# Performance work log

Hardware: AMD Instinct MI355X
Metric: run time of the kernel (lower is better)

The kernel has to match this reference:

```python
import jax, jax.numpy as jnp
import numpy as np
from jax import lax

V, E, H, MEL = 256, 512, 1024, 128
B, T_TXT, T_MEL = 128, 256, 800
BN_EPS = 1e-5


def setup_inputs() -> dict:
    key = jax.random.key(0)
    ks = jax.random.split(key, 32)
    s = 0.05
    n = jax.random.normal
    inp = {
        "x": jax.random.randint(ks[0], (B, T_TXT), 0, V),
        "text_seq_lens": jax.random.randint(ks[1], (B,), 1, T_TXT + 1),
        "y": n(ks[2], (B, T_MEL, MEL), jnp.float32),
        "mel_spec_lens": jax.random.randint(ks[3], (B,), 1, T_MEL + 1),
        # encoder params
        "emb": n(ks[4], (V, E)) * s,
        "enc_lin_W": n(ks[5], (E, E)) * s,
        "enc_lin_b": jnp.zeros((E,)),
        "conv1_W": n(ks[6], (E, E, 3)) * s,
        "conv1_b": jnp.zeros((E,)),
        "bn1_g": 1.0 + n(ks[7], (E,)) * s,
        "bn1_b": n(ks[8], (E,)) * s,
        "conv2_W": n(ks[9], (E, E, 3)) * s,
        "conv2_b": jnp.zeros((E,)),
        "bn2_g": 1.0 + n(ks[10], (E,)) * s,
        "bn2_b": n(ks[11], (E,)) * s,
        # encoder LSTM (torch gate order i,f,g,o); b = b_ih + b_hh fused
        "Wih_e": n(ks[12], (4 * H, E)) * s,
        "Whh_e": n(ks[13], (4 * H, H)) * s,
        "b_e": n(ks[14], (4 * H,)) * 0.01,
        # decoder LSTM
        "Wih_d": n(ks[15], (4 * H, MEL)) * s,
        "Whh_d": n(ks[16], (4 * H, H)) * s,
        "b_d": n(ks[17], (4 * H,)) * 0.01,
        # output projections
        "Wp": n(ks[18], (MEL, H)) * s,
        "bp": jnp.zeros((MEL,)),
        "Wg": n(ks[19], (1, H)) * s,
        "bg": jnp.zeros((1,)),
    }
    return inp


def lstm_step(xt, h, c, Wih, Whh, b):
    g = xt @ Wih.T + h @ Whh.T + b  # [B, 4H]
    i, f, gg, o = jnp.split(g, 4, axis=-1)
    c2 = jax.nn.sigmoid(f) * c + jax.nn.sigmoid(i) * jnp.tanh(gg)
    h2 = jax.nn.sigmoid(o) * jnp.tanh(c2)
    return h2, c2


def reference(x, text_seq_lens, y, mel_spec_lens, emb, enc_lin_W, enc_lin_b,
              conv1_W, conv1_b, bn1_g, bn1_b, conv2_W, conv2_b, bn2_g, bn2_b,
              Wih_e, Whh_e, b_e, Wih_d, Whh_d, b_d, Wp, bp, Wg, bg):
    Bq, Ttxt = x.shape
    Tmel = y.shape[1]
    dt = y.dtype

    def conv_bn_relu(h, W, b, g, beta):
        h = lax.conv_general_dilated(h, W, (1,), ((1, 1),),
                                     dimension_numbers=("NCH", "OIH", "NCH"))
        h = h + b[None, :, None]
        # BN in eval mode: running_mean=0, running_var=1
        h = g[None, :, None] * (h / jnp.sqrt(1.0 + BN_EPS)) + beta[None, :, None]
        return jax.nn.relu(h)  # dropout is identity in eval

    e = emb[x]                                  # [B,T,E]
    e = e @ enc_lin_W.T + enc_lin_b
    h = e.transpose(0, 2, 1)                    # [B,E,T]
    h = conv_bn_relu(h, conv1_W, conv1_b, bn1_g, bn1_b)
    h = conv_bn_relu(h, conv2_W, conv2_b, bn2_g, bn2_b)
    h = h.transpose(0, 2, 1)                    # [B,T,E]

    # encoder LSTM with pack_padded semantics: state frozen past seq len,
    # so final (h,c) is the state at each sequence's true last step.
    valid = jnp.arange(Ttxt)[:, None] < text_seq_lens[None, :]  # [T,B]

    def enc_step(carry, inp):
        hh, cc = carry
        xt, v = inp
        h2, c2 = lstm_step(xt, hh, cc, Wih_e, Whh_e, b_e)
        v = v[:, None]
        return (jnp.where(v, h2, hh), jnp.where(v, c2, cc)), None

    z = jnp.zeros((Bq, H), dt)
    (hS, cS), _ = lax.scan(enc_step, (z, z), (h.transpose(1, 0, 2), valid))

    def dec_step(carry, _):
        hh, cc, inp = carry
        h2, c2 = lstm_step(inp, hh, cc, Wih_d, Whh_d, b_d)
        mel = h2 @ Wp.T + bp           # [B,MEL]
        gate = (h2 @ Wg.T + bg)[:, 0]  # [B]
        return (h2, c2, mel), (mel, gate)

    sos = jnp.zeros((Bq, MEL), dt)
    _, (mels, gates) = lax.scan(dec_step, (hS, cS, sos), None, length=Tmel)
    mels = mels.transpose(1, 0, 2)   # [B,Tmel,MEL]
    gates = gates.T                  # [B,Tmel]

    mask = jnp.arange(Tmel)[None, :] > mel_spec_lens[:, None]  # strict > as in source
    masked_mel = jnp.where(mask[:, :, None], jnp.zeros((), dt), mels)
    masked_gate = jnp.where(mask, jnp.asarray(1000.0, dt), gates)
    return masked_mel, masked_gate, mask
```

## Files before the change

### kernel.cpp

```cpp
#include <hip/hip_runtime.h>
#include <math.h>

#define BB 128
#define TT 256
#define TMEL 800
#define EE 512
#define HH 1024
#define MELD 128
#define VV 256

#define OFF_PROJ  0u
#define OFF_T1    131072u
#define OFF_WR2   524288u
#define OFF_BB1   1310720u
#define OFF_BB2   1311232u
#define OFF_B2    1311744u
#define OFF_W2C   1315840u
#define OFF_BAR   5510144u
#define OFF_WENCR 5522688u
#define OFF_WIHS  7619840u
#define OFF_W2CR  8668416u
#define OFF_WHHDS 10765568u
#define OFF_WPGS  12862720u
#define OFF_H2B   12936448u
#define OFF_RING  21325056u

typedef __bf16 bfv8 __attribute__((ext_vector_type(8)));
typedef float f32x4 __attribute__((ext_vector_type(4)));
typedef unsigned u32x4 __attribute__((ext_vector_type(4)));

__device__ __forceinline__ unsigned short f2b(float f){
  union { float f; unsigned u; } v; v.f = f;
  unsigned u = v.u;
  return (unsigned short)((u + 0x7fffu + ((u>>16)&1u)) >> 16);
}
__device__ __forceinline__ float sigm(float x){ return 1.0f/(1.0f+expf(-x)); }

__device__ __forceinline__ f32x4 mfma16(bfv8 a, bfv8 b, f32x4 c){
  return __builtin_amdgcn_mfma_f32_16x16x32_bf16(a, b, c, 0, 0, 0);
}


__global__ void k_proj(const float* __restrict__ emb, const float* __restrict__ W,
                       const float* __restrict__ bias, float* __restrict__ proj){
  __shared__ float er[EE];
  int v = blockIdx.x;
  for(int i=threadIdx.x;i<EE;i+=256) er[i]=emb[v*EE+i];
  __syncthreads();
  for(int e=threadIdx.x;e<EE;e+=256){
    const float* wr = W + e*EE;
    float acc=0.f;
    for(int k=0;k<EE;k+=4){
      float4 w4 = *(const float4*)(wr+k);
      acc += er[k]*w4.x + er[k+1]*w4.y + er[k+2]*w4.z + er[k+3]*w4.w;
    }
    proj[v*EE+e] = acc + bias[e];
  }
}

__global__ void k_t1(const float* __restrict__ proj, const float* __restrict__ W1,
                     const float* __restrict__ g1, float* __restrict__ T1){
  __shared__ float pr[EE];
  int v = blockIdx.x; int k3 = blockIdx.y;
  for(int i=threadIdx.x;i<EE;i+=256) pr[i]=proj[v*EE+i];
  __syncthreads();
  const float s = rsqrtf(1.f+1e-5f);
  for(int c=threadIdx.x;c<EE;c+=256){
    float acc=0.f;
    const float* w = W1 + c*EE*3 + k3;
    for(int ci=0;ci<EE;ci++) acc += pr[ci]*w[ci*3];
    T1[(v*3+k3)*EE+c] = g1[c]*s*acc;
  }
}

__global__ void k_wr2(const float* __restrict__ W2, const float* __restrict__ g2,
                      unsigned short* __restrict__ Wr){
  int idx = blockIdx.x*256+threadIdx.x;
  if(idx >= EE*3*EE) return;
  int c = idx/1536; int r = idx%1536; int k3 = r/EE; int ci = r%EE;
  const float s = rsqrtf(1.f+1e-5f);
  Wr[idx] = f2b(g2[c]*s*W2[(c*EE+ci)*3+k3]);
}

__global__ void k_bb(const float* __restrict__ b1,const float* __restrict__ g1,const float* __restrict__ be1,
                     const float* __restrict__ b2,const float* __restrict__ g2,const float* __restrict__ be2,
                     float* __restrict__ bb1, float* __restrict__ bb2){
  int c = threadIdx.x + blockIdx.x*256; if(c>=EE) return;
  const float s = rsqrtf(1.f+1e-5f);
  bb1[c] = g1[c]*s*b1[c] + be1[c];
  bb2[c] = g2[c]*s*b2[c] + be2[c];
}

__global__ void k_b2(const float* __restrict__ bd, const float* __restrict__ Wih,
                     const float* __restrict__ bp, float* __restrict__ b2){
  int j = blockIdx.x*256+threadIdx.x; if(j>=4096) return;
  float acc = bd[j];
  const float* w = Wih + j*MELD;
  for(int m=0;m<MELD;m++) acc += w[m]*bp[m];
  b2[j] = acc;
}

__global__ void k_w2c(const float* __restrict__ Whh, const float* __restrict__ Wih,
                      const float* __restrict__ Wp, float* __restrict__ W2c){
  __shared__ float wl[8][MELD];
  int j0 = blockIdx.x*8; int k = blockIdx.y*256 + threadIdx.x;
  for(int i=threadIdx.x;i<8*MELD;i+=256) wl[i/MELD][i%MELD] = Wih[(j0+i/MELD)*MELD + (i%MELD)];
  __syncthreads();
  float acc[8];
  #pragma unroll
  for(int jj=0;jj<8;jj++) acc[jj]=Whh[(j0+jj)*HH+k];
  for(int m=0;m<MELD;m++){
    float wp = Wp[m*HH+k];
    #pragma unroll
    for(int jj=0;jj<8;jj++) acc[jj] += wl[jj][m]*wp;
  }
  #pragma unroll
  for(int jj=0;jj<8;jj++) W2c[(j0+jj)*HH+k] = acc[jj];
}

__global__ void k_pack(const float* __restrict__ src, unsigned short* __restrict__ dst,
                       int NKT, int K){
  int tile = blockIdx.x;
  int cg = tile>>3, wv = tile&7;
  int tot = NKT*64*8;
  for(int i=threadIdx.x; i<tot; i+=256){
    int kt = i>>9; int l = (i>>3)&63; int e = i&7;
    int j = (wv>>1)*1024 + cg*32 + (wv&1)*16 + (l&15);
    int k = ((l>>4)<<3) + kt*32 + e;
    dst[((size_t)(tile*NKT + kt)*64 + l)*8 + e] = f2b(src[(size_t)j*K + k]);
  }
}

__global__ void k_pack_pg(const float* __restrict__ Wp, const float* __restrict__ Wg,
                          unsigned short* __restrict__ dst){
  int nt = blockIdx.x;
  for(int i=threadIdx.x; i<32*64*8; i+=256){
    int kt = i>>9; int l = (i>>3)&63; int e = i&7;
    int n = nt*16 + (l&15);
    int k = ((l>>4)<<3) + kt*32 + e;
    float v = (n<MELD)? Wp[(size_t)n*HH+k] : (n==MELD? Wg[k] : 0.f);
    dst[((size_t)(nt*32 + kt)*64 + l)*8 + e] = f2b(v);
  }
}


__global__ void k_pad(unsigned short* __restrict__ h1pb){
  int idx = blockIdx.x*256+threadIdx.x;
  int c = idx & 511; int b = idx >> 9;
  h1pb[((size_t)b*258)*EE + c] = 0;
  h1pb[((size_t)b*258 + 257)*EE + c] = 0;
}

__global__ void k_conv1(const int* __restrict__ x, const float* __restrict__ T1,
                        const float* __restrict__ bb1, unsigned short* __restrict__ h1pb){
  int idx = blockIdx.x*256+threadIdx.x;
  int c = idx & 511; int bt = idx >> 9; int t = bt & 255; int b = bt >> 8;
  float acc = bb1[c];
  if(t > 0)    acc += T1[(size_t)(x[b*TT+t-1]*3+0)*EE+c];
               acc += T1[(size_t)(x[b*TT+t  ]*3+1)*EE+c];
  if(t < TT-1) acc += T1[(size_t)(x[b*TT+t+1]*3+2)*EE+c];
  h1pb[((size_t)b*258 + t + 1)*EE + c] = f2b(fmaxf(acc, 0.f));
}

template<int NKT>
__device__ __forceinline__ void mm_seg_stream(const unsigned short* A, int lda,
    const unsigned short* Wrow, f32x4& acc0, f32x4& acc1, int l, int wv){
  int r0 = wv*32 + (l&15);
  int k8 = (l>>4)*8;
  const unsigned short* a0 = A + (size_t)r0*lda + k8;
  const unsigned short* a1 = a0 + 16*lda;
  const unsigned short* wp = Wrow + k8;
  #pragma unroll
  for(int kt=0;kt<NKT;kt++){
    bfv8 bv = *(const bfv8*)(const void*)(wp + kt*32);
    acc0 = mfma16(*(const bfv8*)(const void*)(a0 + kt*32), bv, acc0);
    acc1 = mfma16(*(const bfv8*)(const void*)(a1 + kt*32), bv, acc1);
  }
}

__global__ __launch_bounds__(256,2) void k_conv2mm(const unsigned short* __restrict__ h1pb,
    const unsigned short* __restrict__ Wr2b, const float* __restrict__ bb2,
    unsigned short* __restrict__ h2b){
  int b = blockIdx.x;
  int th = blockIdx.y;
  int nt = blockIdx.z;
  int tid=threadIdx.x; int wv=tid>>6, l=tid&63;
  const unsigned short* A = h1pb + ((size_t)b*258 + th*128)*EE;
  const unsigned short* Wrow = Wr2b + (size_t)(nt*16+(l&15))*1536;
  f32x4 acc0={0,0,0,0}, acc1={0,0,0,0};
  mm_seg_stream<48>(A, EE, Wrow, acc0, acc1, l, wv);
  int rr=(l>>4)*4, cc=l&15;
  int n = nt*16+cc;
  float bias = bb2[n];
  #pragma unroll
  for(int mi=0;mi<2;mi++){
    f32x4 acc = mi?acc1:acc0;
    int tb = th*128 + wv*32 + mi*16 + rr;
    #pragma unroll
    for(int q=0;q<4;q++){
      float v = fmaxf(acc[q]+bias, 0.f);
      h2b[((size_t)(tb+q)*BB + b)*EE + n] = f2b(v);
    }
  }
}

__device__ __forceinline__ unsigned l2_poll(unsigned* p){
  unsigned v;
  asm volatile("global_atomic_add %0, %1, %2, off sc0\n\ts_waitcnt vmcnt(0)"
               : "=v"(v) : "v"(p), "v"(0u) : "memory");
  return v;
}

__device__ __forceinline__ void g_arrive(unsigned* cnt_slow, unsigned* gen_slow,
                                         unsigned* cnt_fast, unsigned* bcast_base,
                                         bool fastp){
  __syncthreads();
  if(threadIdx.x == 0){
    if(fastp){
      unsigned old = __hip_atomic_fetch_add(cnt_fast, 1u, __ATOMIC_RELAXED, __HIP_MEMORY_SCOPE_WORKGROUP);
      if((old & 31u) == 31u){
        unsigned g = (old + 1u) >> 5;
        #pragma unroll
        for(int i=0;i<32;i++)
          __hip_atomic_store(bcast_base + i*32, g, __ATOMIC_RELAXED, __HIP_MEMORY_SCOPE_WORKGROUP);
      }
    } else {
      unsigned old = __hip_atomic_fetch_add(cnt_slow, 1u, __ATOMIC_RELAXED, __HIP_MEMORY_SCOPE_AGENT);
      if(old == 31u){
        __hip_atomic_store(cnt_slow, 0u, __ATOMIC_RELAXED, __HIP_MEMORY_SCOPE_AGENT);
        __hip_atomic_fetch_add(gen_slow, 1u, __ATOMIC_RELAXED, __HIP_MEMORY_SCOPE_AGENT);
      }
    }
  }
}
__device__ __forceinline__ void g_wait(unsigned* gen_slow, unsigned* mybcast,
                                       unsigned ge, bool fastp){
  if(threadIdx.x == 0){
    if(fastp){
      while(l2_poll(mybcast) < ge) __builtin_amdgcn_s_sleep(1);
    } else {
      while(__hip_atomic_load(gen_slow, __ATOMIC_RELAXED, __HIP_MEMORY_SCOPE_AGENT) < ge)
        __builtin_amdgcn_s_sleep(1);
    }
  }
  asm volatile("" ::: "memory");
  __syncthreads();
}

__device__ __forceinline__ void h_store(unsigned int* ptr, unsigned int val, bool fastp){
  if(fastp) __hip_atomic_store(ptr, val, __ATOMIC_RELAXED, __HIP_MEMORY_SCOPE_WORKGROUP);
  else      __hip_atomic_store(ptr, val, __ATOMIC_RELAXED, __HIP_MEMORY_SCOPE_AGENT);
}
__device__ __forceinline__ void h_store64(unsigned long long* ptr, unsigned long long val, bool fastp){
  if(fastp) __hip_atomic_store(ptr, val, __ATOMIC_RELAXED, __HIP_MEMORY_SCOPE_WORKGROUP);
  else      __hip_atomic_store(ptr, val, __ATOMIC_RELAXED, __HIP_MEMORY_SCOPE_AGENT);
}

__device__ __forceinline__ void stage_h(unsigned short* hs, const unsigned short* slotp,
                                        int bg, int tid, bool fastp){
  if(fastp){
    const char* base = (const char*)(slotp + (size_t)(bg*16)*HH);
    #pragma unroll
    for(int jj=0;jj<2;jj++){
      int i0 = tid + (jj*2+0)*512, i1 = tid + (jj*2+1)*512;
      int r0 = i0>>7, c0 = i0&127, r1 = i1>>7, c1 = i1&127;
      int o0 = r0*2048 + c0*16,     o1 = r1*2048 + c1*16;
      u32x4 v0, v1;
      asm volatile(
        "global_load_dwordx4 %0, %2, off sc0\n\t"
        "global_load_dwordx4 %1, %3, off sc0\n\t"
        "s_waitcnt vmcnt(0)"
        : "=&v"(v0), "=&v"(v1)
        : "v"(base + o0), "v"(base + o1)
        : "memory");
      *(u32x4*)((char*)hs + (o0 ^ ((r0&7)<<4))) = v0;
      *(u32x4*)((char*)hs + (o1 ^ ((r1&7)<<4))) = v1;
    }
  } else {
    for(int i = tid; i < 4096; i += 512){
      int r = i >> 8, c8 = i & 255;
      const unsigned long long* p =
        (const unsigned long long*)(slotp + (size_t)(bg*16+r)*HH + c8*4);
      unsigned long long v = __hip_atomic_load(p, __ATOMIC_RELAXED, __HIP_MEMORY_SCOPE_AGENT);
      *(unsigned long long*)((char*)hs + ((r*2048 + c8*8) ^ ((r&7)<<4))) = v;
    }
  }
}

__global__ __launch_bounds__(512,1) void k_recur(
  const unsigned short* __restrict__ h2b, unsigned short* __restrict__ ring,
  const unsigned short* __restrict__ WencR, const unsigned short* __restrict__ WihS,
  const unsigned short* __restrict__ W2cR, const unsigned short* __restrict__ WhhdS,
  const unsigned short* __restrict__ WpgS,
  const float* __restrict__ bhe, const float* __restrict__ bd, const float* __restrict__ b2,
  const float* __restrict__ bp, const float* __restrict__ bgp,
  unsigned int* __restrict__ bar,
  const int* __restrict__ tlen, const int* __restrict__ mlen,
  float* __restrict__ outmel, float* __restrict__ outgate)
{
  __shared__ __align__(16) unsigned short hs[16*1024];
  __shared__ __align__(16) unsigned short Xs[16*512];
  __shared__ float Gs[16][132];
  __shared__ unsigned s_ids[32];
  __shared__ int s_fast;

  const int bid = blockIdx.x;
  const int bg = bid & 7, cg = bid >> 3;
  const int tid = threadIdx.x;
  const int wvi = tid >> 6, l = tid & 63;
  const int tile = cg*8 + wvi;
  unsigned int* cnt_slow = bar + bg*32;
  unsigned int* gen_slow = bar + 256 + bg*32;
  unsigned int* xtab     = bar + 512;
  unsigned int* cnt_fast = bar + 1024 + bg*32;
  unsigned int* bcastb   = bar + 2048 + bg*1024;
  unsigned int* mybcast  = bcastb + cg*32;
  unsigned int ge = 0;

  if(tid == 0){
    unsigned id;
    asm volatile("s_getreg_b32 %0, hwreg(HW_REG_XCC_ID)" : "=s"(id));
    __hip_atomic_store(xtab + bid, id + 1u, __ATOMIC_RELAXED, __HIP_MEMORY_SCOPE_AGENT);
  }
  if(tid < 32){
    unsigned v;
    do {
      v = __hip_atomic_load(xtab + (tid*8 + bg), __ATOMIC_RELAXED, __HIP_MEMORY_SCOPE_AGENT);
    } while(v == 0u);
    s_ids[tid] = v;
  }
  __syncthreads();
  if(tid == 0){
    int f = 1;
    for(int i=1;i<32;i++) if(s_ids[i] != s_ids[0]) f = 0;
    s_fast = f;
  }
  __syncthreads();
  const bool fastp = (s_fast != 0);

  const int fr = l & 15;
  const int hswz = (fr & 7) << 4;
  const int hbase = fr*2048 + ((l>>4)<<4);
  const int xbase = fr*1024 + ((l>>4)<<4);

  const int lr = tid >> 4;
  const int lc = (tid & 15) * 2;
  const int hcol = cg*32 + lc;
  float cs0 = 0.f, cs1 = 0.f;
  unsigned int hp = 0u;
  int mylen = 0;
  if(tid < 256) mylen = tlen[bg*16 + lr];

  if(tid < 128){
    int r = tid >> 3, c4 = (tid & 7) * 4;
    unsigned long long* p = (unsigned long long*)
      (ring + (size_t)100*BB*HH + (size_t)(bg*16+r)*HH + cg*32 + c4);
    h_store64(p, 0ull, fastp);
  }
  ge++; g_arrive(cnt_slow, gen_slow, cnt_fast, bcastb, fastp);

  f32x4 bw[32];

  {
    const f32x4* wsrc = (const f32x4*)(const void*)(WencR + ((size_t)(tile*32)*64 + l)*8);
    #pragma unroll
    for(int kt=0;kt<32;kt++) bw[kt] = wsrc[kt*64];
    #pragma unroll
    for(int kt=0;kt<32;kt++) asm volatile("" : "+v"(bw[kt]));
  }

  float ei0=0,ei1=0,ef0=0,ef1=0,eg0=0,eg1=0,eo0=0,eo1=0;
  if(tid < 256){
    ei0=bhe[hcol];      ei1=bhe[hcol+1];
    ef0=bhe[HH+hcol];   ef1=bhe[HH+hcol+1];
    eg0=bhe[2*HH+hcol]; eg1=bhe[2*HH+hcol+1];
    eo0=bhe[3*HH+hcol]; eo1=bhe[3*HH+hcol+1];
  }

  #pragma unroll 1
  for(int t=0;t<TT;t++){
    {
      const uint4* src = (const uint4*)(h2b + (size_t)(t*BB + bg*16)*EE);
      for(int i = tid; i < 1024; i += 512){
        int r = i >> 6, c16 = i & 63;
        uint4 v = src[r*64 + c16];
        *(uint4*)((char*)Xs + ((r*1024 + c16*16) ^ ((r&7)<<4))) = v;
      }
    }
    __syncthreads();
    f32x4 a0 = {0.f,0.f,0.f,0.f}, a1 = {0.f,0.f,0.f,0.f};
    {
      const unsigned short* wsrc = WihS + (size_t)tile*16*64*8;
      #pragma unroll
      for(int kt=0;kt<16;kt+=2){
        bfv8 wf0 = *(const bfv8*)(const void*)(wsrc + ((size_t)kt*64 + l)*8);
        bfv8 wf1 = *(const bfv8*)(const void*)(wsrc + ((size_t)(kt+1)*64 + l)*8);
        bfv8 xv0 = *(const bfv8*)(const void*)((const char*)Xs + ((xbase + kt*64) ^ hswz));
        bfv8 xv1 = *(const bfv8*)(const void*)((const char*)Xs + ((xbase + (kt+1)*64) ^ hswz));
        a0 = mfma16(xv0, wf0, a0);
        a1 = mfma16(xv1, wf1, a1);
      }
    }
    g_wait(gen_slow, mybcast, ge, fastp);
    stage_h(hs, ring + (size_t)(100 + (t&1))*BB*HH, bg, tid, fastp);
    __syncthreads();
    #pragma unroll
    for(int kt=0;kt<32;kt+=2){
      bfv8 hv0 = *(const bfv8*)(const void*)((const char*)hs + ((hbase + kt*64) ^ hswz));
      bfv8 hv1 = *(const bfv8*)(const void*)((const char*)hs + ((hbase + (kt+1)*64) ^ hswz));
      a0 = mfma16(hv0, __builtin_bit_cast(bfv8, bw[kt]), a0);
      a1 = mfma16(hv1, __builtin_bit_cast(bfv8, bw[kt+1]), a1);
    }
    {
      f32x4 acc = a0 + a1;
      int rr = (l>>4)*4;
      #pragma unroll
      for(int q=0;q<4;q++) Gs[rr+q][wvi*16 + fr] = acc[q];
    }
    __syncthreads();
    if(tid < 256){
      float gi0 = Gs[lr][lc]    + ei0, gi1 = Gs[lr][lc+1] + ei1;
      float gf0 = Gs[lr][32+lc] + ef0, gf1 = Gs[lr][33+lc] + ef1;
      float gg0 = Gs[lr][64+lc] + eg0, gg1 = Gs[lr][65+lc] + eg1;
      float go0 = Gs[lr][96+lc] + eo0, go1 = Gs[lr][97+lc] + eo1;
      float c20 = sigm(gf0)*cs0 + sigm(gi0)*tanhf(gg0);
      float c21 = sigm(gf1)*cs1 + sigm(gi1)*tanhf(gg1);
      float h20 = sigm(go0)*tanhf(c20);
      float h21 = sigm(go1)*tanhf(c21);
      if(t < mylen){
        cs0 = c20; cs1 = c21;
        hp = (unsigned)f2b(h20) | ((unsigned)f2b(h21)<<16);
      }
      unsigned short* outslot = (t==TT-1) ? (ring + (size_t)99*BB*HH)
                                          : (ring + (size_t)(100 + ((t+1)&1))*BB*HH);
      h_store((unsigned int*)(outslot + (size_t)(bg*16+lr)*HH + hcol), hp, fastp);
    }
    ge++; g_arrive(cnt_slow, gen_slow, cnt_fast, bcastb, fastp);
  }

  {
    const f32x4* wsrc = (const f32x4*)(const void*)(W2cR + ((size_t)(tile*32)*64 + l)*8);
    #pragma unroll
    for(int kt=0;kt<32;kt++) bw[kt] = wsrc[kt*64];
    #pragma unroll
    for(int kt=0;kt<32;kt++) asm volatile("" : "+v"(bw[kt]));
  }

  float di0=0,di1=0,df0=0,df1=0,dg0=0,dg1=0,do0=0,do1=0;
  if(tid < 256){
    di0=b2[hcol];      di1=b2[hcol+1];
    df0=b2[HH+hcol];   df1=b2[HH+hcol+1];
    dg0=b2[2*HH+hcol]; dg1=b2[2*HH+hcol+1];
    do0=b2[3*HH+hcol]; do1=b2[3*HH+hcol+1];
  }

  #pragma unroll 1
  for(int t=0;t<TMEL;t++){
    g_wait(gen_slow, mybcast, ge, fastp);
    const unsigned short* slotin = (t==0) ? ring + (size_t)99*BB*HH
                                          : ring + (size_t)((t-1)%100)*BB*HH;
    stage_h(hs, slotin, bg, tid, fastp);
    __syncthreads();
    f32x4 a0 = {0.f,0.f,0.f,0.f}, a1 = {0.f,0.f,0.f,0.f};
    if(t == 0){
      const unsigned short* wsrc = WhhdS + (size_t)tile*32*64*8;
      #pragma unroll
      for(int kt=0;kt<32;kt+=2){
        bfv8 wf0 = *(const bfv8*)(const void*)(wsrc + ((size_t)kt*64 + l)*8);
        bfv8 wf1 = *(const bfv8*)(const void*)(wsrc + ((size_t)(kt+1)*64 + l)*8);
        bfv8 hv0 = *(const bfv8*)(const void*)((const char*)hs + ((hbase + kt*64) ^ hswz));
        bfv8 hv1 = *(const bfv8*)(const void*)((const char*)hs + ((hbase + (kt+1)*64) ^ hswz));
        a0 = mfma16(hv0, wf0, a0);
        a1 = mfma16(hv1, wf1, a1);
      }
    } else {
      #pragma unroll
      for(int kt=0;kt<32;kt+=2){
        bfv8 hv0 = *(const bfv8*)(const void*)((const char*)hs + ((hbase + kt*64) ^ hswz));
        bfv8 hv1 = *(const bfv8*)(const void*)((const char*)hs + ((hbase + (kt+1)*64) ^ hswz));
        a0 = mfma16(hv0, __builtin_bit_cast(bfv8, bw[kt]), a0);
        a1 = mfma16(hv1, __builtin_bit_cast(bfv8, bw[kt+1]), a1);
      }
    }
    {
      f32x4 acc = a0 + a1;
      int rr = (l>>4)*4;
      #pragma unroll
      for(int q=0;q<4;q++) Gs[rr+q][wvi*16 + fr] = acc[q];
    }
    __syncthreads();
    if(tid < 256){
      float bi0=di0,bi1=di1,bf0=df0,bf1=df1,bg0=dg0,bg1=dg1,bo0=do0,bo1=do1;
      if(t==0){
        bi0=bd[hcol];      bi1=bd[hcol+1];
        bf0=bd[HH+hcol];   bf1=bd[HH+hcol+1];
        bg0=bd[2*HH+hcol]; bg1=bd[2*HH+hcol+1];
        bo0=bd[3*HH+hcol]; bo1=bd[3*HH+hcol+1];
      }
      float gi0 = Gs[lr][lc]    + bi0, gi1 = Gs[lr][lc+1] + bi1;
      float gf0 = Gs[lr][32+lc] + bf0, gf1 = Gs[lr][33+lc] + bf1;
      float gg0 = Gs[lr][64+lc] + bg0, gg1 = Gs[lr][65+lc] + bg1;
      float go0 = Gs[lr][96+lc] + bo0, go1 = Gs[lr][97+lc] + bo1;
      float c20 = sigm(gf0)*cs0 + sigm(gi0)*tanhf(gg0);
      float c21 = sigm(gf1)*cs1 + sigm(gi1)*tanhf(gg1);
      cs0 = c20; cs1 = c21;
      float h20 = sigm(go0)*tanhf(c20);
      float h21 = sigm(go1)*tanhf(c21);
      unsigned int hn = (unsigned)f2b(h20) | ((unsigned)f2b(h21)<<16);
      unsigned short* outslot = ring + (size_t)(t%100)*BB*HH;
      h_store((unsigned int*)(outslot + (size_t)(bg*16+lr)*HH + hcol), hn, fastp);
    }
    ge++; g_arrive(cnt_slow, gen_slow, cnt_fast, bcastb, fastp);

    if((t%100)==99){
      g_wait(gen_slow, mybcast, ge, fastp);
      int tbase = t - 99;
      #pragma unroll 1
      for(int s = cg; s < 100; s += 32){
        stage_h(hs, ring + (size_t)s*BB*HH, bg, tid, fastp);
        __syncthreads();
        int tout = tbase + s;
        #pragma unroll 1
        for(int pass=0; pass<2; pass++){
          int nt = (pass==0) ? wvi : 8;
          if(pass==1 && wvi!=0) break;
          const unsigned short* wsrc = WpgS + (size_t)nt*32*64*8;
          f32x4 acc = {0.f,0.f,0.f,0.f};
          #pragma unroll
          for(int kt=0;kt<32;kt++){
            bfv8 wf = *(const bfv8*)(const void*)(wsrc + ((size_t)kt*64 + l)*8);
            bfv8 hv = *(const bfv8*)(const void*)((const char*)hs + ((hbase + kt*64) ^ hswz));
            acc = mfma16(hv, wf, acc);
          }
          int n = nt*16 + fr;
          #pragma unroll
          for(int q=0;q<4;q++){
            int b = bg*16 + (l>>4)*4 + q;
            bool msk = tout > mlen[b];
            if(n < MELD)
              outmel[((size_t)b*TMEL + tout)*MELD + n] = msk ? 0.f : acc[q]+bp[n];
            else if(n == MELD)
              outgate[(size_t)b*TMEL + tout] = msk ? 1000.f : acc[q]+bgp[0];
          }
        }
        __syncthreads();
      }
      ge++; g_arrive(cnt_slow, gen_slow, cnt_fast, bcastb, fastp);
    }
  }
}

__global__ void k_mask(const int* __restrict__ mlen, float* __restrict__ om){
  int idx=blockIdx.x*256+threadIdx.x; if(idx>=BB*TMEL) return;
  int b=idx/TMEL, t=idx%TMEL;
  om[idx] = (t > mlen[b]) ? 1.f : 0.f;
}

extern "C" void kernel_launch(void* const* d_in, const int* in_sizes, int n_in,
                              void* d_out, int out_size, void* d_ws, size_t ws_size,
                              hipStream_t stream){
  (void)in_sizes; (void)n_in; (void)out_size; (void)ws_size;
  const int*   x    = (const int*)d_in[0];
  const int*   tlen = (const int*)d_in[1];
  const int*   mlen = (const int*)d_in[3];
  const float* emb  = (const float*)d_in[4];
  const float* elW  = (const float*)d_in[5];
  const float* elb  = (const float*)d_in[6];
  const float* c1W  = (const float*)d_in[7];
  const float* c1b  = (const float*)d_in[8];
  const float* g1   = (const float*)d_in[9];
  const float* be1  = (const float*)d_in[10];
  const float* c2W  = (const float*)d_in[11];
  const float* c2b  = (const float*)d_in[12];
  const float* g2   = (const float*)d_in[13];
  const float* be2  = (const float*)d_in[14];
  const float* Wihe = (const float*)d_in[15];
  const float* Whhe = (const float*)d_in[16];
  const float* bhe  = (const float*)d_in[17];
  const float* Wihd = (const float*)d_in[18];
  const float* Whhd = (const float*)d_in[19];
  const float* bhd  = (const float*)d_in[20];
  const float* Wp   = (const float*)d_in[21];
  const float* bp   = (const float*)d_in[22];
  const float* Wg   = (const float*)d_in[23];
  const float* bg   = (const float*)d_in[24];

  float* ws = (float*)d_ws;
  float* proj = ws + OFF_PROJ;
  float* T1   = ws + OFF_T1;
  unsigned short* Wr2b = (unsigned short*)(ws + OFF_WR2);
  float* bb1 = ws + OFF_BB1;
  float* bb2 = ws + OFF_BB2;
  float* b2  = ws + OFF_B2;
  float* W2c = ws + OFF_W2C;
  unsigned int* bar = (unsigned int*)(ws + OFF_BAR);
  unsigned short* WencR = (unsigned short*)(ws + OFF_WENCR);
  unsigned short* WihS  = (unsigned short*)(ws + OFF_WIHS);
  unsigned short* W2cR  = (unsigned short*)(ws + OFF_W2CR);
  unsigned short* WhhdS = (unsigned short*)(ws + OFF_WHHDS);
  unsigned short* WpgS  = (unsigned short*)(ws + OFF_WPGS);
  unsigned short* h2b   = (unsigned short*)(ws + OFF_H2B);
  unsigned short* h1pb  = (unsigned short*)(ws + OFF_RING);
  unsigned short* ring  = (unsigned short*)(ws + OFF_RING);

  float* outmel  = (float*)d_out;
  float* outgate = outmel + (size_t)BB*TMEL*MELD;
  float* outmask = outgate + (size_t)BB*TMEL;

  hipMemsetAsync(bar, 0, 40960, stream);

  k_proj<<<VV,256,0,stream>>>(emb, elW, elb, proj);
  k_t1<<<dim3(VV,3),256,0,stream>>>(proj, c1W, g1, T1);
  k_wr2<<<(EE*3*EE+255)/256,256,0,stream>>>(c2W, g2, Wr2b);
  k_bb<<<2,256,0,stream>>>(c1b,g1,be1,c2b,g2,be2,bb1,bb2);
  k_b2<<<16,256,0,stream>>>(bhd, Wihd, bp, b2);
  k_w2c<<<dim3(4096/8,HH/256),256,0,stream>>>(Whhd, Wihd, Wp, W2c);
  k_pack<<<256,256,0,stream>>>(Whhe, WencR, 32, 1024);
  k_pack<<<256,256,0,stream>>>(Wihe, WihS, 16, 512);
  k_pack<<<256,256,0,stream>>>(W2c,  W2cR, 32, 1024);
  k_pack<<<256,256,0,stream>>>(Whhd, WhhdS, 32, 1024);
  k_pack_pg<<<9,256,0,stream>>>(Wp, Wg, WpgS);
  k_pad<<<256,256,0,stream>>>(h1pb);
  k_conv1<<<65536,256,0,stream>>>(x, T1, bb1, h1pb);
  k_conv2mm<<<dim3(BB,2,32),256,0,stream>>>(h1pb, Wr2b, bb2, h2b);

  void* kargs[] = {
    (void*)&h2b, (void*)&ring, (void*)&WencR, (void*)&WihS, (void*)&W2cR, (void*)&WhhdS,
    (void*)&WpgS, (void*)&bhe, (void*)&bhd, (void*)&b2, (void*)&bp, (void*)&bg,
    (void*)&bar, (void*)&tlen, (void*)&mlen, (void*)&outmel, (void*)&outgate
  };
  hipLaunchCooperativeKernel((void*)k_recur, dim3(256), dim3(512), kargs, 0u, stream);

  k_mask<<<(BB*TMEL+255)/256,256,0,stream>>>(mlen, outmask);
}
```

Before: 7.795 ms.

## Repack gate weights so each wave owns complete LSTM gates, using shuffles instead of LDS

The packed weight layout is permuted so that each wave's 16 MFMA output columns hold the i, f, g and o gates for the same 4 hidden units. The LSTM cell update can then be done in-wave with shuffles instead of staging gates through a shared-memory tile and an extra __syncthreads per step. It also merges the h staging loads into a single batch of four outstanding global loads before one wait. In exchange, all 512 threads now do redundant transcendental math and only a quarter of lanes issue stores, and the cell state is spread across four registers per lane.

```diff
diff --git a/kernel.cpp b/kernel.cpp
--- a/kernel.cpp
+++ b/kernel.cpp
@@ -125,7 +125,8 @@
   int tot = NKT*64*8;
   for(int i=threadIdx.x; i<tot; i+=256){
     int kt = i>>9; int l = (i>>3)&63; int e = i&7;
-    int j = (wv>>1)*1024 + cg*32 + (wv&1)*16 + (l&15);
+    int c = l & 15;
+    int j = (c>>2)*1024 + cg*32 + wv*4 + (c&3);
     int k = ((l>>4)<<3) + kt*32 + e;
     dst[((size_t)(tile*NKT + kt)*64 + l)*8 + e] = f2b(src[(size_t)j*K + k]);
   }
@@ -260,22 +261,28 @@
                                         int bg, int tid, bool fastp){
   if(fastp){
     const char* base = (const char*)(slotp + (size_t)(bg*16)*HH);
-    #pragma unroll
-    for(int jj=0;jj<2;jj++){
-      int i0 = tid + (jj*2+0)*512, i1 = tid + (jj*2+1)*512;
-      int r0 = i0>>7, c0 = i0&127, r1 = i1>>7, c1 = i1&127;
-      int o0 = r0*2048 + c0*16,     o1 = r1*2048 + c1*16;
-      u32x4 v0, v1;
-      asm volatile(
-        "global_load_dwordx4 %0, %2, off sc0\n\t"
-        "global_load_dwordx4 %1, %3, off sc0\n\t"
-        "s_waitcnt vmcnt(0)"
-        : "=&v"(v0), "=&v"(v1)
-        : "v"(base + o0), "v"(base + o1)
-        : "memory");
-      *(u32x4*)((char*)hs + (o0 ^ ((r0&7)<<4))) = v0;
-      *(u32x4*)((char*)hs + (o1 ^ ((r1&7)<<4))) = v1;
-    }
+    int o[4]; const void* p[4];
+    #pragma unroll
+    for(int jj=0;jj<4;jj++){
+      int i = tid + jj*512;
+      int r = i>>7, cc = i&127;
+      o[jj] = r*2048 + cc*16;
+      p[jj] = base + o[jj];
+    }
+    u32x4 v0,v1,v2,v3;
+    asm volatile(
+      "global_load_dwordx4 %0, %4, off sc0\n\t"
+      "global_load_dwordx4 %1, %5, off sc0\n\t"
+      "global_load_dwordx4 %2, %6, off sc0\n\t"
+      "global_load_dwordx4 %3, %7, off sc0\n\t"
+      "s_waitcnt vmcnt(0)"
+      : "=&v"(v0), "=&v"(v1), "=&v"(v2), "=&v"(v3)
+      : "v"(p[0]), "v"(p[1]), "v"(p[2]), "v"(p[3])
+      : "memory");
+    *(u32x4*)((char*)hs + (o[0] ^ (((o[0]>>11)&7)<<4))) = v0;
+    *(u32x4*)((char*)hs + (o[1] ^ (((o[1]>>11)&7)<<4))) = v1;
+    *(u32x4*)((char*)hs + (o[2] ^ (((o[2]>>11)&7)<<4))) = v2;
+    *(u32x4*)((char*)hs + (o[3] ^ (((o[3]>>11)&7)<<4))) = v3;
   } else {
     for(int i = tid; i < 4096; i += 512){
       int r = i >> 8, c8 = i & 255;
@@ -300,7 +307,6 @@
 {
   __shared__ __align__(16) unsigned short hs[16*1024];
   __shared__ __align__(16) unsigned short Xs[16*512];
-  __shared__ float Gs[16][132];
   __shared__ unsigned s_ids[32];
   __shared__ int s_fast;
 
@@ -343,13 +349,17 @@
   const int hbase = fr*2048 + ((l>>4)<<4);
   const int xbase = fr*1024 + ((l>>4)<<4);
 
-  const int lr = tid >> 4;
-  const int lc = (tid & 15) * 2;
-  const int hcol = cg*32 + lc;
-  float cs0 = 0.f, cs1 = 0.f;
-  unsigned int hp = 0u;
-  int mylen = 0;
-  if(tid < 256) mylen = tlen[bg*16 + lr];
+  const int c15 = l & 15;
+  const int jh = c15 & 3;
+  const int jcol = (c15>>2)*HH + cg*32 + wvi*4 + jh;
+  const int shbase = l & 48;
+  const bool storer = (c15 == 0) | (c15 == 2);
+
+  float cs[4] = {0.f,0.f,0.f,0.f};
+  float hpr[4] = {0.f,0.f,0.f,0.f};
+  int tl4[4];
+  #pragma unroll
+  for(int q=0;q<4;q++) tl4[q] = tlen[bg*16 + (l>>4)*4 + q];
 
   if(tid < 128){
     int r = tid >> 3, c4 = (tid & 7) * 4;
@@ -368,14 +378,7 @@
     #pragma unroll
     for(int kt=0;kt<32;kt++) asm volatile("" : "+v"(bw[kt]));
   }
-
-  float ei0=0,ei1=0,ef0=0,ef1=0,eg0=0,eg1=0,eo0=0,eo1=0;
-  if(tid < 256){
-    ei0=bhe[hcol];      ei1=bhe[hcol+1];
-    ef0=bhe[HH+hcol];   ef1=bhe[HH+hcol+1];
-    eg0=bhe[2*HH+hcol]; eg1=bhe[2*HH+hcol+1];
-    eo0=bhe[3*HH+hcol]; eo1=bhe[3*HH+hcol+1];
-  }
+  float ebias = bhe[jcol];
 
   #pragma unroll 1
   for(int t=0;t<TT;t++){
@@ -411,29 +414,26 @@
       a0 = mfma16(hv0, __builtin_bit_cast(bfv8, bw[kt]), a0);
       a1 = mfma16(hv1, __builtin_bit_cast(bfv8, bw[kt+1]), a1);
     }
-    {
-      f32x4 acc = a0 + a1;
-      int rr = (l>>4)*4;
-      #pragma unroll
-      for(int q=0;q<4;q++) Gs[rr+q][wvi*16 + fr] = acc[q];
-    }
-    __syncthreads();
-    if(tid < 256){
-      float gi0 = Gs[lr][lc]    + ei0, gi1 = Gs[lr][lc+1] + ei1;
-      float gf0 = Gs[lr][32+lc] + ef0, gf1 = Gs[lr][33+lc] + ef1;
-      float gg0 = Gs[lr][64+lc] + eg0, gg1 = Gs[lr][65+lc] + eg1;
-      float go0 = Gs[lr][96+lc] + eo0, go1 = Gs[lr][97+lc] + eo1;
-      float c20 = sigm(gf0)*cs0 + sigm(gi0)*tanhf(gg0);
-      float c21 = sigm(gf1)*cs1 + sigm(gi1)*tanhf(gg1);
-      float h20 = sigm(go0)*tanhf(c20);
-      float h21 = sigm(go1)*tanhf(c21);
-      if(t < mylen){
-        cs0 = c20; cs1 = c21;
-        hp = (unsigned)f2b(h20) | ((unsigned)f2b(h21)<<16);
-      }
-      unsigned short* outslot = (t==TT-1) ? (ring + (size_t)99*BB*HH)
-                                          : (ring + (size_t)(100 + ((t+1)&1))*BB*HH);
-      h_store((unsigned int*)(outslot + (size_t)(bg*16+lr)*HH + hcol), hp, fastp);
+    f32x4 g4 = a0 + a1;
+    #pragma unroll
+    for(int q=0;q<4;q++) g4[q] += ebias;
+    unsigned short* outslot = (t==TT-1) ? (ring + (size_t)99*BB*HH)
+                                        : (ring + (size_t)(100 + ((t+1)&1))*BB*HH);
+    #pragma unroll
+    for(int q=0;q<4;q++){
+      float gi = __shfl(g4[q], shbase + jh);
+      float gf = __shfl(g4[q], shbase + 4 + jh);
+      float gg = __shfl(g4[q], shbase + 8 + jh);
+      float go = __shfl(g4[q], shbase + 12 + jh);
+      float c2 = sigm(gf)*cs[q] + sigm(gi)*tanhf(gg);
+      float h2 = sigm(go)*tanhf(c2);
+      if(t < tl4[q]){ cs[q] = c2; hpr[q] = h2; }
+      float po = __shfl(hpr[q], shbase + (c15^1));
+      if(storer){
+        unsigned pk = (unsigned)f2b(hpr[q]) | ((unsigned)f2b(po)<<16);
+        h_store((unsigned int*)(outslot + (size_t)(bg*16 + (l>>4)*4 + q)*HH
+                                + cg*32 + wvi*4 + c15), pk, fastp);
+      }
     }
     ge++; g_arrive(cnt_slow, gen_slow, cnt_fast, bcastb, fastp);
   }
@@ -445,14 +445,8 @@
     #pragma unroll
     for(int kt=0;kt<32;kt++) asm volatile("" : "+v"(bw[kt]));
   }
-
-  float di0=0,di1=0,df0=0,df1=0,dg0=0,dg1=0,do0=0,do1=0;
-  if(tid < 256){
-    di0=b2[hcol];      di1=b2[hcol+1];
-    df0=b2[HH+hcol];   df1=b2[HH+hcol+1];
-    dg0=b2[2*HH+hcol]; dg1=b2[2*HH+hcol+1];
-    do0=b2[3*HH+hcol]; do1=b2[3*HH+hcol+1];
-  }
+  float db2 = b2[jcol];
+  float dbd = bd[jcol];
 
   #pragma unroll 1
   for(int t=0;t<TMEL;t++){
@@ -482,33 +476,26 @@
         a1 = mfma16(hv1, __builtin_bit_cast(bfv8, bw[kt+1]), a1);
       }
     }
-    {
-      f32x4 acc = a0 + a1;
-      int rr = (l>>4)*4;
-      #pragma unroll
-      for(int q=0;q<4;q++) Gs[rr+q][wvi*16 + fr] = acc[q];
-    }
-    __syncthreads();
-    if(tid < 256){
-      float bi0=di0,bi1=di1,bf0=df0,bf1=df1,bg0=dg0,bg1=dg1,bo0=do0,bo1=do1;
-      if(t==0){
-        bi0=bd[hcol];      bi1=bd[hcol+1];
-        bf0=bd[HH+hcol];   bf1=bd[HH+hcol+1];
-        bg0=bd[2*HH+hcol]; bg1=bd[2*HH+hcol+1];
-        bo0=bd[3*HH+hcol]; bo1=bd[3*HH+hcol+1];
-      }
-      float gi0 = Gs[lr][lc]    + bi0, gi1 = Gs[lr][lc+1] + bi1;
-      float gf0 = Gs[lr][32+lc] + bf0, gf1 = Gs[lr][33+lc] + bf1;
-      float gg0 = Gs[lr][64+lc] + bg0, gg1 = Gs[lr][65+lc] + bg1;
-      float go0 = Gs[lr][96+lc] + bo0, go1 = Gs[lr][97+lc] + bo1;
-      float c20 = sigm(gf0)*cs0 + sigm(gi0)*tanhf(gg0);
-      float c21 = sigm(gf1)*cs1 + sigm(gi1)*tanhf(gg1);
-      cs0 = c20; cs1 = c21;
-      float h20 = sigm(go0)*tanhf(c20);
-      float h21 = sigm(go1)*tanhf(c21);
-      unsigned int hn = (unsigned)f2b(h20) | ((unsigned)f2b(h21)<<16);
-      unsigned short* outslot = ring + (size_t)(t%100)*BB*HH;
-      h_store((unsigned int*)(outslot + (size_t)(bg*16+lr)*HH + hcol), hn, fastp);
+    f32x4 g4 = a0 + a1;
+    float bb = (t==0) ? dbd : db2;
+    #pragma unroll
+    for(int q=0;q<4;q++) g4[q] += bb;
+    unsigned short* outslot = ring + (size_t)(t%100)*BB*HH;
+    #pragma unroll
+    for(int q=0;q<4;q++){
+      float gi = __shfl(g4[q], shbase + jh);
+      float gf = __shfl(g4[q], shbase + 4 + jh);
+      float gg = __shfl(g4[q], shbase + 8 + jh);
+      float go = __shfl(g4[q], shbase + 12 + jh);
+      float c2 = sigm(gf)*cs[q] + sigm(gi)*tanhf(gg);
+      float h2 = sigm(go)*tanhf(c2);
+      cs[q] = c2; hpr[q] = h2;
+      float po = __shfl(hpr[q], shbase + (c15^1));
+      if(storer){
+        unsigned pk = (unsigned)f2b(hpr[q]) | ((unsigned)f2b(po)<<16);
+        h_store((unsigned int*)(outslot + (size_t)(bg*16 + (l>>4)*4 + q)*HH
+                                + cg*32 + wvi*4 + c15), pk, fastp);
+      }
     }
     ge++; g_arrive(cnt_slow, gen_slow, cnt_fast, bcastb, fastp);
 
```

Result: slower. 10.42 ms (+33.7%).
